# Kernel optimization log

Measured on AMD Instinct MI355X. Metric: run time of the kernel, lower is better.

Reference implementation:

```python
import jax, jax.numpy as jnp
import numpy as np

STRIDE = 1  # conv stride from __init__


def setup_inputs() -> dict:
    key = jax.random.key(0)
    k1, k2, k3 = jax.random.split(key, 3)
    prot1 = jax.random.normal(k1, (4, 1024, 8, 64), dtype=jnp.float32)
    prot2 = jax.random.normal(k2, (4, 1024, 8, 64), dtype=jnp.float32)
    # W: (no_filters, no_channels, no_dims, window_size)
    W = jax.random.normal(k3, (32, 8, 64, 7), dtype=jnp.float32)
    return {"prot1": prot1, "prot2": prot2, "W": W}


def _project(x, W, stride):
    """Fused equivalent of unfold + broadcast-mul + sum over (C, window).

    x: (N, H, C, D), W: (F, C, D, w) -> (N, F, H', D) with H' = (H - w)//stride + 1.
    This is a grouped 1D conv: D groups, each mixing C input channels into F outputs.
    """
    N, H, C, D = x.shape
    Fn, _, _, w = W.shape
    xg = jnp.transpose(x, (0, 3, 2, 1)).reshape(N, D * C, H)        # (N, D*C, H)
    Wg = jnp.transpose(W, (2, 0, 1, 3)).reshape(D * Fn, C, w)       # (D*F, C, w)
    out = jax.lax.conv_general_dilated(
        xg, Wg, window_strides=(stride,), padding='VALID',
        dimension_numbers=('NCH', 'OIH', 'NCH'), feature_group_count=D)
    Hp = out.shape[-1]
    return jnp.transpose(out.reshape(N, D, Fn, Hp), (0, 2, 3, 1))   # (N, F, H', D)


def reference(prot1, prot2, W):
    q1 = _project(prot1, W, STRIDE)   # (N, F, H1', D)
    q2 = _project(prot2, W, STRIDE)   # (N, F, H2', D)
    H1p, H2p = q1.shape[2], q2.shape[2]
    scale = jnp.sqrt(jnp.asarray(H1p * H2p, dtype=q1.dtype))
    att = jnp.einsum('nfhd,nfgd->nfhg', q1, q2) / scale             # (N, F, H1', H2')
    a = jax.nn.softmax(att, axis=3)
    p1 = jnp.einsum('nfhg,nfgd->nfhd', a, q2)                       # (N, F, H1', D)
    # NB: source does transpose(att, 2, 2) (a no-op) and multiplies the SAME
    # softmax matrix by the UPDATED p1folds; we reproduce that faithfully.
    p2 = jnp.einsum('nfhg,nfgd->nfhd', a, p1)                       # (N, F, H1', D)
    out1 = jnp.tanh(jnp.transpose(p1, (0, 2, 1, 3)))                # (N, H1', F, D)
    out2 = jnp.tanh(jnp.transpose(p2, (0, 2, 1, 3)))
    # Dropout is identity in eval mode (and dropout_p=0.0 here).
    return (out1, out2)
```

## Files before the change

### kernel.cpp

```cpp
#include <hip/hip_runtime.h>
#include <math.h>

typedef __bf16 bf16_t;
typedef bf16_t bf16x4 __attribute__((ext_vector_type(4)));
typedef bf16_t bf16x8 __attribute__((ext_vector_type(8)));
typedef float  f32x16 __attribute__((ext_vector_type(16)));

#define HH 1024
#define CC 8
#define DD 64
#define FF 32
#define WW 7
#define HP 1018
#define HPAD 1024
#define NF 128
#define QOUT (NF*HP*DD)
#define QWS ((size_t)NF*HPAD*DD)

#if __has_builtin(__builtin_amdgcn_exp2f)
#define EXP2(x) __builtin_amdgcn_exp2f(x)
#else
#define EXP2(x) __expf((x) * 0.6931471805599453f)
#endif

__device__ __forceinline__ int vaddr(int row, int col) {
    return row*64 + ((((col>>3) ^ (row&7) ^ ((row>>2)&7)))<<3) + (col&7);
}

__global__ __launch_bounds__(256) void wprep_kernel(
    const float* __restrict__ Wt, float* __restrict__ Wp)
{
    const int idx = blockIdx.x * 256 + threadIdx.x;
    if (idx < FF*CC*DD*WW) {
        const int j = idx % WW;
        int t = idx / WW;
        const int d = t % DD; t /= DD;
        const int c = t % CC;
        const int f = t / CC;
        Wp[((f*CC + c)*WW + j)*DD + d] = Wt[idx];
    }
}

__global__ __launch_bounds__(256) void conv_kernel(
    const float* __restrict__ x1, const float* __restrict__ x2,
    const float* __restrict__ Wp, bf16_t* __restrict__ q1, bf16_t* __restrict__ q2)
{
    __shared__ float xs[38*512];
    const float* x = blockIdx.z ? x2 : x1;
    bf16_t* q = blockIdx.z ? q2 : q1;
    const int n = blockIdx.y;
    const int hb = blockIdx.x * 32;
    const int tid = threadIdx.x;

    const float4* xg = (const float4*)(x + (size_t)n*HH*512);
    for (int i = tid; i < 38*128; i += 256) {
        const int row = hb + (i >> 7);
        float4 v = {0.f, 0.f, 0.f, 0.f};
        if (row < HH) v = xg[(size_t)row*128 + (i & 127)];
        const int r = i >> 7;
        const int c = (i & 127) >> 4;
        const int d0 = ((i & 127) & 15) * 4;
        xs[r*512 + (d0+0)*8 + c] = v.x;
        xs[r*512 + (d0+1)*8 + c] = v.y;
        xs[r*512 + (d0+2)*8 + c] = v.z;
        xs[r*512 + (d0+3)*8 + c] = v.w;
    }
    __syncthreads();

    const int d = tid & 63;
    const int fq = tid >> 6;
    for (int fi = 0; fi < 8; ++fi) {
        const int f = fq*8 + fi;
        float w[CC][WW];
#pragma unroll
        for (int c = 0; c < CC; ++c)
#pragma unroll
            for (int j = 0; j < WW; ++j)
                w[c][j] = Wp[((f*CC + c)*WW + j)*DD + d];
#pragma unroll
        for (int hc = 0; hc < 2; ++hc) {
            float acc[16];
#pragma unroll
            for (int i = 0; i < 16; ++i) acc[i] = 0.f;
#pragma unroll
            for (int rr = 0; rr < 22; ++rr) {
                const float4 a = *(const float4*)&xs[(hc*16 + rr)*512 + d*8 + 0];
                const float4 b = *(const float4*)&xs[(hc*16 + rr)*512 + d*8 + 4];
                const float xv[8] = {a.x, a.y, a.z, a.w, b.x, b.y, b.z, b.w};
#pragma unroll
                for (int j = 0; j < WW; ++j) {
                    const int i = rr - j;
                    if (i >= 0 && i < 16) {
#pragma unroll
                        for (int c = 0; c < CC; ++c)
                            acc[i] = fmaf(xv[c], w[c][j], acc[i]);
                    }
                }
            }
#pragma unroll
            for (int i = 0; i < 16; ++i) {
                const int h = hb + hc*16 + i;
                const float v = (h < HP) ? acc[i] : 0.f;
                q[((size_t)(n*FF + f)*HPAD + h)*DD + d] = (bf16_t)v;
            }
        }
    }
}

__device__ __forceinline__ float fast_tanh(float x) {
    const float t = __expf(2.f * x);
    return (t - 1.f) / (t + 1.f);
}

template<int MODE>
__global__ __launch_bounds__(256, 2) void flash(
    const bf16_t* __restrict__ q1, const bf16_t* __restrict__ q2,
    const bf16_t* __restrict__ vsrc, bf16_t* __restrict__ p1out,
    float* __restrict__ out)
{
    __shared__ __align__(16) bf16_t Vt[64*64];

    const int head = blockIdx.y;
    const int n = head >> 5, f = head & 31;
    const int tid = threadIdx.x;
    const int w = tid >> 6;
    const int lane = tid & 63;
    const int lid = lane & 31;
    const int half = lane >> 5;
    const int hb = blockIdx.x * 256 + w * 64;

    const size_t qoff = (size_t)head * HPAD * DD;
    const float SC = 1.442695041f / 1018.f;
    const int vswz = (lid & 7) ^ (lid >> 2);

    const int gq = tid >> 4;
    const int dq = tid & 15;
    const int cgb = 4*((gq>>1)&1) + 8*(gq&1) + 16*(gq>>2);

    const bf16_t* vptr = (MODE == 1) ? vsrc : q2;

    bf16x8 bq1[2][4];
#pragma unroll
    for (int nt = 0; nt < 2; ++nt)
#pragma unroll
        for (int kt = 0; kt < 4; ++kt)
            bq1[nt][kt] = *(const bf16x8*)&q1[qoff + (size_t)(hb + 32*nt + lid)*DD + 16*kt + 8*half];

    bf16x8 aq[2][4];
#pragma unroll
    for (int mt = 0; mt < 2; ++mt)
#pragma unroll
        for (int kt = 0; kt < 4; ++kt)
            aq[mt][kt] = *(const bf16x8*)&q2[qoff + (size_t)(32*mt + lid)*DD + 16*kt + 8*half];

    bf16x4 rV[4];
#pragma unroll
    for (int i = 0; i < 4; ++i)
        rV[i] = *(const bf16x4*)&vptr[qoff + (size_t)(4*gq + i)*DD + 4*dq];

    f32x16 O[2][2] = {};
    float lacc[2] = {0.f, 0.f};

    for (int g0 = 0; g0 < HPAD; g0 += 64) {
        __syncthreads();
#pragma unroll
        for (int j = 0; j < 4; ++j) {
            bf16x4 c = { rV[0][j], rV[1][j], rV[2][j], rV[3][j] };
            *(bf16x4*)&Vt[vaddr(4*dq + j, cgb)] = c;
        }
        __syncthreads();

        if (g0 + 64 < HPAD) {
#pragma unroll
            for (int i = 0; i < 4; ++i)
                rV[i] = *(const bf16x4*)&vptr[qoff + (size_t)(g0 + 64 + 4*gq + i)*DD + 4*dq];
        }

        const bool tail = (g0 + 64 > HP);

#pragma unroll
        for (int mt = 0; mt < 2; ++mt) {
            f32x16 C[2] = {};
#pragma unroll
            for (int kt = 0; kt < 4; ++kt) {
                C[0] = __builtin_amdgcn_mfma_f32_32x32x16_bf16(aq[mt][kt], bq1[0][kt], C[0], 0,0,0);
                C[1] = __builtin_amdgcn_mfma_f32_32x32x16_bf16(aq[mt][kt], bq1[1][kt], C[1], 0,0,0);
            }
            if (g0 + 64 < HPAD) {
#pragma unroll
                for (int kt = 0; kt < 4; ++kt)
                    aq[mt][kt] = *(const bf16x8*)&q2[qoff + (size_t)(g0 + 64 + 32*mt + lid)*DD + 16*kt + 8*half];
            }
            bf16x8 af[2][2];
#pragma unroll
            for (int nt = 0; nt < 2; ++nt) {
                float ls = 0.f;
#pragma unroll
                for (int s = 0; s < 16; ++s) {
                    float e = EXP2(C[nt][s] * SC);
                    if (tail) {
                        const int gg = g0 + 32*mt + (s&3) + 8*(s>>2) + 4*half;
                        if (gg >= HP) e = 0.f;
                    }
                    ls += e;
                    af[nt][s>>3][s&7] = (bf16_t)e;
                }
                lacc[nt] += ls;
            }
#pragma unroll
            for (int u = 0; u < 2; ++u) {
#pragma unroll
                for (int dt = 0; dt < 2; ++dt) {
                    const int chunk = (4*mt + 2*u + half) ^ vswz;
                    bf16x8 b = *(const bf16x8*)&Vt[(32*dt + lid)*64 + chunk*8];
                    O[0][dt] = __builtin_amdgcn_mfma_f32_32x32x16_bf16(af[0][u], b, O[0][dt], 0,0,0);
                    O[1][dt] = __builtin_amdgcn_mfma_f32_32x32x16_bf16(af[1][u], b, O[1][dt], 0,0,0);
                }
            }
        }
    }

    float linv[2];
#pragma unroll
    for (int nt = 0; nt < 2; ++nt) {
        const float l = lacc[nt] + __shfl_xor(lacc[nt], 32);
        linv[nt] = 1.f / l;
    }
#pragma unroll
    for (int ht = 0; ht < 2; ++ht) {
#pragma unroll
        for (int s = 0; s < 16; ++s) {
            const int R = (s&3) + 8*(s>>2) + 4*half;
            const float li = __shfl(linv[ht], R);
            const int hg = hb + 32*ht + R;
#pragma unroll
            for (int dt = 0; dt < 2; ++dt) {
                const int d = 32*dt + lid;
                const float val = O[ht][dt][s] * li;
                if (hg < HP)
                    out[(((size_t)n*HP + hg)*FF + f)*DD + d] = fast_tanh(val);
                if (MODE == 0)
                    p1out[qoff + (size_t)hg*DD + d] = (bf16_t)(hg < HP ? val : 0.f);
            }
        }
    }
}

extern "C" void kernel_launch(void* const* d_in, const int* in_sizes, int n_in,
                              void* d_out, int out_size, void* d_ws, size_t ws_size,
                              hipStream_t stream)
{
    const float* prot1 = (const float*)d_in[0];
    const float* prot2 = (const float*)d_in[1];
    const float* Wt    = (const float*)d_in[2];
    float* out = (float*)d_out;

    bf16_t* q1b = (bf16_t*)d_ws;
    bf16_t* q2b = q1b + QWS;
    bf16_t* p1b = q2b + QWS;
    float* Wp   = (float*)(p1b + QWS);

    wprep_kernel<<<dim3(448), 256, 0, stream>>>(Wt, Wp);
    conv_kernel<<<dim3(32, 4, 2), 256, 0, stream>>>(prot1, prot2, Wp, q1b, q2b);
    flash<0><<<dim3(4, NF), 256, 0, stream>>>(q1b, q2b, q2b, p1b, out);
    flash<1><<<dim3(4, NF), 256, 0, stream>>>(q1b, q2b, p1b, p1b, out + QOUT);
}
```

Before: 219.9 us.

## Halve per-wave query tile, double flash/conv grids, fold softmax scale into q1

The flash kernels now give each wave 32 query rows instead of 64, doubling the grid to 8x128 blocks and raising launch bounds to 4 blocks per SM for more occupancy. The conv kernel splits the filter loop across an extra grid dimension to double its block count. The softmax scale (log2e/1018) is folded into q1 when it is written out in bf16, which removes a multiply per score. In exchange, each q2/V tile is reloaded by twice as many blocks, and pre-scaling q1 before the bf16 cast slightly changes rounding.

```diff
diff --git a/kernel.cpp b/kernel.cpp
--- a/kernel.cpp
+++ b/kernel.cpp
@@ -23,6 +23,8 @@
 #define EXP2(x) __expf((x) * 0.6931471805599453f)
 #endif
 
+#define QSCALE (1.442695040888963f / 1018.f)
+
 __device__ __forceinline__ int vaddr(int row, int col) {
     return row*64 + ((((col>>3) ^ (row&7) ^ ((row>>2)&7)))<<3) + (col&7);
 }
@@ -46,8 +48,11 @@
     const float* __restrict__ Wp, bf16_t* __restrict__ q1, bf16_t* __restrict__ q2)
 {
     __shared__ float xs[38*512];
-    const float* x = blockIdx.z ? x2 : x1;
-    bf16_t* q = blockIdx.z ? q2 : q1;
+    const int zin = blockIdx.z & 1;
+    const int fh = blockIdx.z >> 1;
+    const float* x = zin ? x2 : x1;
+    bf16_t* q = zin ? q2 : q1;
+    const float qs = zin ? 1.f : QSCALE;
     const int n = blockIdx.y;
     const int hb = blockIdx.x * 32;
     const int tid = threadIdx.x;
@@ -69,8 +74,8 @@
 
     const int d = tid & 63;
     const int fq = tid >> 6;
-    for (int fi = 0; fi < 8; ++fi) {
-        const int f = fq*8 + fi;
+    for (int fi = 0; fi < 4; ++fi) {
+        const int f = fq*8 + fh*4 + fi;
         float w[CC][WW];
 #pragma unroll
         for (int c = 0; c < CC; ++c)
@@ -100,7 +105,7 @@
 #pragma unroll
             for (int i = 0; i < 16; ++i) {
                 const int h = hb + hc*16 + i;
-                const float v = (h < HP) ? acc[i] : 0.f;
+                const float v = (h < HP) ? acc[i]*qs : 0.f;
                 q[((size_t)(n*FF + f)*HPAD + h)*DD + d] = (bf16_t)v;
             }
         }
@@ -113,7 +118,7 @@
 }
 
 template<int MODE>
-__global__ __launch_bounds__(256, 2) void flash(
+__global__ __launch_bounds__(256, 4) void flash(
     const bf16_t* __restrict__ q1, const bf16_t* __restrict__ q2,
     const bf16_t* __restrict__ vsrc, bf16_t* __restrict__ p1out,
     float* __restrict__ out)
@@ -127,10 +132,9 @@
     const int lane = tid & 63;
     const int lid = lane & 31;
     const int half = lane >> 5;
-    const int hb = blockIdx.x * 256 + w * 64;
+    const int hb = blockIdx.x * 128 + w * 32;
 
     const size_t qoff = (size_t)head * HPAD * DD;
-    const float SC = 1.442695041f / 1018.f;
     const int vswz = (lid & 7) ^ (lid >> 2);
 
     const int gq = tid >> 4;
@@ -139,27 +143,29 @@
 
     const bf16_t* vptr = (MODE == 1) ? vsrc : q2;
 
-    bf16x8 bq1[2][4];
-#pragma unroll
-    for (int nt = 0; nt < 2; ++nt)
+    const bf16_t* bp = q1 + qoff + (size_t)(hb + lid)*DD + 8*half;
+    const bf16_t* ap = q2 + qoff + (size_t)lid*DD + 8*half;
+    const bf16_t* vp = vptr + qoff + (size_t)(4*gq)*DD + 4*dq;
+
+    bf16x8 bq1[4];
+#pragma unroll
+    for (int kt = 0; kt < 4; ++kt)
+        bq1[kt] = *(const bf16x8*)&bp[16*kt];
+
+    bf16x8 aq[2][4];
+#pragma unroll
+    for (int mt = 0; mt < 2; ++mt)
 #pragma unroll
         for (int kt = 0; kt < 4; ++kt)
-            bq1[nt][kt] = *(const bf16x8*)&q1[qoff + (size_t)(hb + 32*nt + lid)*DD + 16*kt + 8*half];
-
-    bf16x8 aq[2][4];
-#pragma unroll
-    for (int mt = 0; mt < 2; ++mt)
-#pragma unroll
-        for (int kt = 0; kt < 4; ++kt)
-            aq[mt][kt] = *(const bf16x8*)&q2[qoff + (size_t)(32*mt + lid)*DD + 16*kt + 8*half];
+            aq[mt][kt] = *(const bf16x8*)&ap[(size_t)(32*mt)*DD + 16*kt];
 
     bf16x4 rV[4];
 #pragma unroll
     for (int i = 0; i < 4; ++i)
-        rV[i] = *(const bf16x4*)&vptr[qoff + (size_t)(4*gq + i)*DD + 4*dq];
-
-    f32x16 O[2][2] = {};
-    float lacc[2] = {0.f, 0.f};
+        rV[i] = *(const bf16x4*)&vp[(size_t)i*DD];
+
+    f32x16 O[2] = {};
+    float lacc = 0.f;
 
     for (int g0 = 0; g0 < HPAD; g0 += 64) {
         __syncthreads();
@@ -173,75 +179,62 @@
         if (g0 + 64 < HPAD) {
 #pragma unroll
             for (int i = 0; i < 4; ++i)
-                rV[i] = *(const bf16x4*)&vptr[qoff + (size_t)(g0 + 64 + 4*gq + i)*DD + 4*dq];
+                rV[i] = *(const bf16x4*)&vp[(size_t)(g0 + 64 + i)*DD];
         }
 
         const bool tail = (g0 + 64 > HP);
 
 #pragma unroll
         for (int mt = 0; mt < 2; ++mt) {
-            f32x16 C[2] = {};
-#pragma unroll
-            for (int kt = 0; kt < 4; ++kt) {
-                C[0] = __builtin_amdgcn_mfma_f32_32x32x16_bf16(aq[mt][kt], bq1[0][kt], C[0], 0,0,0);
-                C[1] = __builtin_amdgcn_mfma_f32_32x32x16_bf16(aq[mt][kt], bq1[1][kt], C[1], 0,0,0);
-            }
+            f32x16 C = {};
+#pragma unroll
+            for (int kt = 0; kt < 4; ++kt)
+                C = __builtin_amdgcn_mfma_f32_32x32x16_bf16(aq[mt][kt], bq1[kt], C, 0,0,0);
             if (g0 + 64 < HPAD) {
 #pragma unroll
                 for (int kt = 0; kt < 4; ++kt)
-                    aq[mt][kt] = *(const bf16x8*)&q2[qoff + (size_t)(g0 + 64 + 32*mt + lid)*DD + 16*kt + 8*half];
-            }
-            bf16x8 af[2][2];
-#pragma unroll
-            for (int nt = 0; nt < 2; ++nt) {
-                float ls = 0.f;
-#pragma unroll
-                for (int s = 0; s < 16; ++s) {
-                    float e = EXP2(C[nt][s] * SC);
-                    if (tail) {
-                        const int gg = g0 + 32*mt + (s&3) + 8*(s>>2) + 4*half;
-                        if (gg >= HP) e = 0.f;
-                    }
-                    ls += e;
-                    af[nt][s>>3][s&7] = (bf16_t)e;
+                    aq[mt][kt] = *(const bf16x8*)&ap[(size_t)(g0 + 64 + 32*mt)*DD + 16*kt];
+            }
+            bf16x8 af[2];
+            float ls = 0.f;
+#pragma unroll
+            for (int s = 0; s < 16; ++s) {
+                float e = EXP2(C[s]);
+                if (tail) {
+                    const int gg = g0 + 32*mt + (s&3) + 8*(s>>2) + 4*half;
+                    if (gg >= HP) e = 0.f;
                 }
-                lacc[nt] += ls;
-            }
+                ls += e;
+                af[s>>3][s&7] = (bf16_t)e;
+            }
+            lacc += ls;
 #pragma unroll
             for (int u = 0; u < 2; ++u) {
 #pragma unroll
                 for (int dt = 0; dt < 2; ++dt) {
                     const int chunk = (4*mt + 2*u + half) ^ vswz;
                     bf16x8 b = *(const bf16x8*)&Vt[(32*dt + lid)*64 + chunk*8];
-                    O[0][dt] = __builtin_amdgcn_mfma_f32_32x32x16_bf16(af[0][u], b, O[0][dt], 0,0,0);
-                    O[1][dt] = __builtin_amdgcn_mfma_f32_32x32x16_bf16(af[1][u], b, O[1][dt], 0,0,0);
+                    O[dt] = __builtin_amdgcn_mfma_f32_32x32x16_bf16(af[u], b, O[dt], 0,0,0);
                 }
             }
         }
     }
 
-    float linv[2];
-#pragma unroll
-    for (int nt = 0; nt < 2; ++nt) {
-        const float l = lacc[nt] + __shfl_xor(lacc[nt], 32);
-        linv[nt] = 1.f / l;
-    }
-#pragma unroll
-    for (int ht = 0; ht < 2; ++ht) {
-#pragma unroll
-        for (int s = 0; s < 16; ++s) {
-            const int R = (s&3) + 8*(s>>2) + 4*half;
-            const float li = __shfl(linv[ht], R);
-            const int hg = hb + 32*ht + R;
-#pragma unroll
-            for (int dt = 0; dt < 2; ++dt) {
-                const int d = 32*dt + lid;
-                const float val = O[ht][dt][s] * li;
-                if (hg < HP)
-                    out[(((size_t)n*HP + hg)*FF + f)*DD + d] = fast_tanh(val);
-                if (MODE == 0)
-                    p1out[qoff + (size_t)hg*DD + d] = (bf16_t)(hg < HP ? val : 0.f);
-            }
+    const float l = lacc + __shfl_xor(lacc, 32);
+    const float linv = 1.f / l;
+#pragma unroll
+    for (int s = 0; s < 16; ++s) {
+        const int R = (s&3) + 8*(s>>2) + 4*half;
+        const float li = __shfl(linv, R);
+        const int hg = hb + R;
+#pragma unroll
+        for (int dt = 0; dt < 2; ++dt) {
+            const int d = 32*dt + lid;
+            const float val = O[dt][s] * li;
+            if (hg < HP)
+                out[(((size_t)n*HP + hg)*FF + f)*DD + d] = fast_tanh(val);
+            if (MODE == 0)
+                p1out[qoff + (size_t)hg*DD + d] = (bf16_t)(hg < HP ? val : 0.f);
         }
     }
 }
@@ -261,7 +254,7 @@
     float* Wp   = (float*)(p1b + QWS);
 
     wprep_kernel<<<dim3(448), 256, 0, stream>>>(Wt, Wp);
-    conv_kernel<<<dim3(32, 4, 2), 256, 0, stream>>>(prot1, prot2, Wp, q1b, q2b);
-    flash<0><<<dim3(4, NF), 256, 0, stream>>>(q1b, q2b, q2b, p1b, out);
-    flash<1><<<dim3(4, NF), 256, 0, stream>>>(q1b, q2b, p1b, p1b, out + QOUT);
-}
+    conv_kernel<<<dim3(32, 4, 4), 256, 0, stream>>>(prot1, prot2, Wp, q1b, q2b);
+    flash<0><<<dim3(8, NF), 256, 0, stream>>>(q1b, q2b, q2b, p1b, out);
+    flash<1><<<dim3(8, NF), 256, 0, stream>>>(q1b, q2b, p1b, p1b, out + QOUT);
+}
```

Measured after the change: 273.1 us. +24.2%, slower.

## Double-buffer V tile in flash kernel, fold softmax scale into conv, split conv filters

Applied to the files above, without the earlier changes.

The flash kernel now double-buffers the transposed V tile in shared memory, so each iteration needs one barrier instead of two, and the write of the next tile overlaps compute on the current one. The softmax scale (log2e/1018) is folded into q1 when the conv kernel writes it, which removes a multiply per exp. The conv grid doubles along z so each block computes half the filters, giving more parallelism. MFMA sections are wrapped in s_setprio. Pre-scaling q1 before the bf16 rounding slightly changes the rounding behaviour, and the extra shared-memory buffer may reduce occupancy.

```diff
diff --git a/kernel.cpp b/kernel.cpp
--- a/kernel.cpp
+++ b/kernel.cpp
@@ -23,6 +23,8 @@
 #define EXP2(x) __expf((x) * 0.6931471805599453f)
 #endif
 
+#define QSCALE (1.442695040888963f / 1018.f)
+
 __device__ __forceinline__ int vaddr(int row, int col) {
     return row*64 + ((((col>>3) ^ (row&7) ^ ((row>>2)&7)))<<3) + (col&7);
 }
@@ -46,8 +48,11 @@
     const float* __restrict__ Wp, bf16_t* __restrict__ q1, bf16_t* __restrict__ q2)
 {
     __shared__ float xs[38*512];
-    const float* x = blockIdx.z ? x2 : x1;
-    bf16_t* q = blockIdx.z ? q2 : q1;
+    const int zin = blockIdx.z & 1;
+    const int fh = blockIdx.z >> 1;
+    const float* x = zin ? x2 : x1;
+    bf16_t* q = zin ? q2 : q1;
+    const float qs = zin ? 1.f : QSCALE;
     const int n = blockIdx.y;
     const int hb = blockIdx.x * 32;
     const int tid = threadIdx.x;
@@ -69,8 +74,8 @@
 
     const int d = tid & 63;
     const int fq = tid >> 6;
-    for (int fi = 0; fi < 8; ++fi) {
-        const int f = fq*8 + fi;
+    for (int fi = 0; fi < 4; ++fi) {
+        const int f = fq*8 + fh*4 + fi;
         float w[CC][WW];
 #pragma unroll
         for (int c = 0; c < CC; ++c)
@@ -100,7 +105,7 @@
 #pragma unroll
             for (int i = 0; i < 16; ++i) {
                 const int h = hb + hc*16 + i;
-                const float v = (h < HP) ? acc[i] : 0.f;
+                const float v = (h < HP) ? acc[i]*qs : 0.f;
                 q[((size_t)(n*FF + f)*HPAD + h)*DD + d] = (bf16_t)v;
             }
         }
@@ -118,7 +123,7 @@
     const bf16_t* __restrict__ vsrc, bf16_t* __restrict__ p1out,
     float* __restrict__ out)
 {
-    __shared__ __align__(16) bf16_t Vt[64*64];
+    __shared__ __align__(16) bf16_t Vt[2][64*64];
 
     const int head = blockIdx.y;
     const int n = head >> 5, f = head & 31;
@@ -130,7 +135,6 @@
     const int hb = blockIdx.x * 256 + w * 64;
 
     const size_t qoff = (size_t)head * HPAD * DD;
-    const float SC = 1.442695041f / 1018.f;
     const int vswz = (lid & 7) ^ (lid >> 2);
 
     const int gq = tid >> 4;
@@ -139,41 +143,58 @@
 
     const bf16_t* vptr = (MODE == 1) ? vsrc : q2;
 
+    const bf16_t* bp = q1 + qoff + (size_t)(hb + lid)*DD + 8*half;
+    const bf16_t* ap = q2 + qoff + (size_t)lid*DD + 8*half;
+    const bf16_t* vp = vptr + qoff + (size_t)(4*gq)*DD + 4*dq;
+
     bf16x8 bq1[2][4];
 #pragma unroll
     for (int nt = 0; nt < 2; ++nt)
 #pragma unroll
         for (int kt = 0; kt < 4; ++kt)
-            bq1[nt][kt] = *(const bf16x8*)&q1[qoff + (size_t)(hb + 32*nt + lid)*DD + 16*kt + 8*half];
+            bq1[nt][kt] = *(const bf16x8*)&bp[(size_t)(32*nt)*DD + 16*kt];
 
     bf16x8 aq[2][4];
 #pragma unroll
     for (int mt = 0; mt < 2; ++mt)
 #pragma unroll
         for (int kt = 0; kt < 4; ++kt)
-            aq[mt][kt] = *(const bf16x8*)&q2[qoff + (size_t)(32*mt + lid)*DD + 16*kt + 8*half];
+            aq[mt][kt] = *(const bf16x8*)&ap[(size_t)(32*mt)*DD + 16*kt];
 
     bf16x4 rV[4];
 #pragma unroll
     for (int i = 0; i < 4; ++i)
-        rV[i] = *(const bf16x4*)&vptr[qoff + (size_t)(4*gq + i)*DD + 4*dq];
+        rV[i] = *(const bf16x4*)&vp[(size_t)i*DD];
+#pragma unroll
+    for (int j = 0; j < 4; ++j) {
+        bf16x4 c = { rV[0][j], rV[1][j], rV[2][j], rV[3][j] };
+        *(bf16x4*)&Vt[0][vaddr(4*dq + j, cgb)] = c;
+    }
+#pragma unroll
+    for (int i = 0; i < 4; ++i)
+        rV[i] = *(const bf16x4*)&vp[(size_t)(64 + i)*DD];
 
     f32x16 O[2][2] = {};
     float lacc[2] = {0.f, 0.f};
 
-    for (int g0 = 0; g0 < HPAD; g0 += 64) {
-        __syncthreads();
-#pragma unroll
-        for (int j = 0; j < 4; ++j) {
-            bf16x4 c = { rV[0][j], rV[1][j], rV[2][j], rV[3][j] };
-            *(bf16x4*)&Vt[vaddr(4*dq + j, cgb)] = c;
-        }
-        __syncthreads();
-
-        if (g0 + 64 < HPAD) {
-#pragma unroll
-            for (int i = 0; i < 4; ++i)
-                rV[i] = *(const bf16x4*)&vptr[qoff + (size_t)(g0 + 64 + 4*gq + i)*DD + 4*dq];
+    __syncthreads();
+
+    for (int t = 0; t < 16; ++t) {
+        const int g0 = t << 6;
+        const bf16_t* vtc = Vt[t & 1];
+
+        if (t + 1 < 16) {
+            bf16_t* vtn = Vt[(t + 1) & 1];
+#pragma unroll
+            for (int j = 0; j < 4; ++j) {
+                bf16x4 c = { rV[0][j], rV[1][j], rV[2][j], rV[3][j] };
+                *(bf16x4*)&vtn[vaddr(4*dq + j, cgb)] = c;
+            }
+            if (t + 2 < 16) {
+#pragma unroll
+                for (int i = 0; i < 4; ++i)
+                    rV[i] = *(const bf16x4*)&vp[(size_t)((t + 2)*64 + i)*DD];
+            }
         }
 
         const bool tail = (g0 + 64 > HP);
@@ -181,15 +202,17 @@
 #pragma unroll
         for (int mt = 0; mt < 2; ++mt) {
             f32x16 C[2] = {};
+            __builtin_amdgcn_s_setprio(1);
 #pragma unroll
             for (int kt = 0; kt < 4; ++kt) {
                 C[0] = __builtin_amdgcn_mfma_f32_32x32x16_bf16(aq[mt][kt], bq1[0][kt], C[0], 0,0,0);
                 C[1] = __builtin_amdgcn_mfma_f32_32x32x16_bf16(aq[mt][kt], bq1[1][kt], C[1], 0,0,0);
             }
+            __builtin_amdgcn_s_setprio(0);
             if (g0 + 64 < HPAD) {
 #pragma unroll
                 for (int kt = 0; kt < 4; ++kt)
-                    aq[mt][kt] = *(const bf16x8*)&q2[qoff + (size_t)(g0 + 64 + 32*mt + lid)*DD + 16*kt + 8*half];
+                    aq[mt][kt] = *(const bf16x8*)&ap[(size_t)(g0 + 64 + 32*mt)*DD + 16*kt];
             }
             bf16x8 af[2][2];
 #pragma unroll
@@ -197,7 +220,7 @@
                 float ls = 0.f;
 #pragma unroll
                 for (int s = 0; s < 16; ++s) {
-                    float e = EXP2(C[nt][s] * SC);
+                    float e = EXP2(C[nt][s]);
                     if (tail) {
                         const int gg = g0 + 32*mt + (s&3) + 8*(s>>2) + 4*half;
                         if (gg >= HP) e = 0.f;
@@ -207,17 +230,20 @@
                 }
                 lacc[nt] += ls;
             }
+            __builtin_amdgcn_s_setprio(1);
 #pragma unroll
             for (int u = 0; u < 2; ++u) {
 #pragma unroll
                 for (int dt = 0; dt < 2; ++dt) {
                     const int chunk = (4*mt + 2*u + half) ^ vswz;
-                    bf16x8 b = *(const bf16x8*)&Vt[(32*dt + lid)*64 + chunk*8];
+                    bf16x8 b = *(const bf16x8*)&vtc[(32*dt + lid)*64 + chunk*8];
                     O[0][dt] = __builtin_amdgcn_mfma_f32_32x32x16_bf16(af[0][u], b, O[0][dt], 0,0,0);
                     O[1][dt] = __builtin_amdgcn_mfma_f32_32x32x16_bf16(af[1][u], b, O[1][dt], 0,0,0);
                 }
             }
-        }
+            __builtin_amdgcn_s_setprio(0);
+        }
+        __syncthreads();
     }
 
     float linv[2];
@@ -261,7 +287,7 @@
     float* Wp   = (float*)(p1b + QWS);
 
     wprep_kernel<<<dim3(448), 256, 0, stream>>>(Wt, Wp);
-    conv_kernel<<<dim3(32, 4, 2), 256, 0, stream>>>(prot1, prot2, Wp, q1b, q2b);
+    conv_kernel<<<dim3(32, 4, 4), 256, 0, stream>>>(prot1, prot2, Wp, q1b, q2b);
     flash<0><<<dim3(4, NF), 256, 0, stream>>>(q1b, q2b, q2b, p1b, out);
     flash<1><<<dim3(4, NF), 256, 0, stream>>>(q1b, q2b, p1b, p1b, out + QOUT);
 }
```

Result: no change. 222.6 us (+1.2%).
